# Performance work log

Measured on AMD Instinct MI355X. Metric: run time of the kernel, lower is better.

The kernel has to match this reference:

```python
import jax, jax.numpy as jnp
import numpy as np

N_NODES = 50000
N_EDGES = 800000
IN_F = 128
HID_F = 128
OUT_F = 128

def safediv(a, b):
    b = jnp.where(b == 0, jnp.ones_like(b), b)
    return a / b

def setup_inputs() -> dict:
    key = jax.random.key(0)
    ks = jax.random.split(key, 8)
    h = jax.random.normal(ks[0], (N_NODES, IN_F), dtype=jnp.float32)
    ppr_weight = jax.random.uniform(ks[1], (N_EDGES,), dtype=jnp.float32)
    Qw = jax.random.normal(ks[2], (HID_F, IN_F), dtype=jnp.float32) * (1.0 / np.sqrt(IN_F))
    Qb = jnp.zeros((HID_F,), dtype=jnp.float32)
    Ww = jax.random.normal(ks[3], (OUT_F, IN_F + HID_F), dtype=jnp.float32) * (1.0 / np.sqrt(IN_F + HID_F))
    Wb = jnp.zeros((OUT_F,), dtype=jnp.float32)
    src = jax.random.randint(ks[4], (N_EDGES,), 0, N_NODES, dtype=jnp.int64 if jax.config.jax_enable_x64 else jnp.int32)
    dst = jax.random.randint(ks[5], (N_EDGES,), 0, N_NODES, dtype=jnp.int64 if jax.config.jax_enable_x64 else jnp.int32)
    return {"h": h, "ppr_weight": ppr_weight, "Qw": Qw, "Qb": Qb, "Ww": Ww, "Wb": Wb, "src": src, "dst": dst}

def reference(h, ppr_weight, Qw, Qb, Ww, Wb, src, dst):
    # neighbor transform: Q(h) -> [N, HID_F]
    hq = h @ Qw.T + Qb
    # message: h_w = hq[src] * ppr_weight  (edge-weighted gather) [E, HID_F]
    msg = hq[src] * ppr_weight[:, None]
    # reduce: scatter-sum messages and weights onto dst nodes
    h_agg = jax.ops.segment_sum(msg, dst, num_segments=N_NODES)
    w = jax.ops.segment_sum(ppr_weight, dst, num_segments=N_NODES)
    # apply: PPR-weighted mean, concat, linear, leaky_relu, L2 normalize
    h_agg = safediv(h_agg, w[:, None])
    h_concat = jnp.concatenate([h, h_agg], axis=1)
    h_new = jax.nn.leaky_relu(h_concat @ Ww.T + Wb, negative_slope=0.01)
    norm = jnp.linalg.norm(h_new, axis=1, keepdims=True)
    return safediv(h_new, norm)
```

## Files before the change

kernel.cpp:

```cpp
#include <hip/hip_runtime.h>
#include <stdint.h>

#define N_NODES 50000
#define N_EDGES 800000
#define IN_F 128
#define HID_F 128
#define OUT_F 128
#define CAT_F 256

#define NB 256
#define CHUNK 3136
#define NBUCK 3125
#define BCAP 384

typedef __bf16 bf16x8 __attribute__((ext_vector_type(8)));
typedef float f32x4 __attribute__((ext_vector_type(4)));

__device__ __forceinline__ uint32_t f2b(float f) {
  uint32_t u = __float_as_uint(f);
  return (u + 0x7fffu + ((u >> 16) & 1u)) >> 16;
}

__global__ void __launch_bounds__(256) prep_hist_kernel(
    const int* __restrict__ dst, int* __restrict__ G, const float* __restrict__ h,
    const float* __restrict__ Qw, const float* __restrict__ Ww, uint16_t* __restrict__ hB,
    uint16_t* __restrict__ QwB, uint16_t* __restrict__ WwB) {
  if (blockIdx.x < NB) {
    __shared__ int hist[NBUCK];
    for (int k = threadIdx.x; k < NBUCK; k += 256) hist[k] = 0;
    __syncthreads();
    int b = blockIdx.x;
    int base = b * CHUNK;
    int end = (base + CHUNK < N_EDGES) ? (base + CHUNK) : N_EDGES;
    for (int i4 = base / 4 + threadIdx.x; i4 * 4 < end; i4 += 256) {
      int4 d4 = ((const int4*)dst)[i4];
      atomicAdd(&hist[d4.x >> 4], 1);
      atomicAdd(&hist[d4.y >> 4], 1);
      atomicAdd(&hist[d4.z >> 4], 1);
      atomicAdd(&hist[d4.w >> 4], 1);
    }
    __syncthreads();
    for (int k = threadIdx.x; k < NBUCK; k += 256) G[(size_t)b * NBUCK + k] = hist[k];
  } else {
    const int TOT4 = (N_NODES * IN_F + HID_F * IN_F + OUT_F * CAT_F) / 4;
    int i4 = (blockIdx.x - NB) * 256 + threadIdx.x;
    if (i4 >= TOT4) return;
    int base = i4 * 4;
    const float* src;
    uint16_t* dstp;
    int off;
    if (base < N_NODES * IN_F) {
      src = h; dstp = hB; off = base;
    } else if (base < N_NODES * IN_F + HID_F * IN_F) {
      src = Qw; dstp = QwB; off = base - N_NODES * IN_F;
    } else {
      src = Ww; dstp = WwB; off = base - N_NODES * IN_F - HID_F * IN_F;
    }
    float4 v = *(const float4*)(src + off);
    ushort4 o;
    o.x = (uint16_t)f2b(v.x); o.y = (uint16_t)f2b(v.y);
    o.z = (uint16_t)f2b(v.z); o.w = (uint16_t)f2b(v.w);
    *(ushort4*)(dstp + off) = o;
  }
}

__global__ void __launch_bounds__(256) colscan_kernel(int* __restrict__ G,
                                                      int* __restrict__ Btot) {
  int w = (blockIdx.x * 256 + (int)threadIdx.x) >> 6;
  if (w >= NBUCK) return;
  int lane = threadIdx.x & 63;
  int v0 = G[(size_t)(4 * lane + 0) * NBUCK + w];
  int v1 = G[(size_t)(4 * lane + 1) * NBUCK + w];
  int v2 = G[(size_t)(4 * lane + 2) * NBUCK + w];
  int v3 = G[(size_t)(4 * lane + 3) * NBUCK + w];
  int s = v0 + v1 + v2 + v3;
  int inc = s;
#pragma unroll
  for (int d = 1; d < 64; d <<= 1) {
    int x = __shfl_up(inc, d, 64);
    if (lane >= d) inc += x;
  }
  int exc = inc - s;
  G[(size_t)(4 * lane + 0) * NBUCK + w] = exc;
  G[(size_t)(4 * lane + 1) * NBUCK + w] = exc + v0;
  G[(size_t)(4 * lane + 2) * NBUCK + w] = exc + v0 + v1;
  G[(size_t)(4 * lane + 3) * NBUCK + w] = exc + v0 + v1 + v2;
  if (lane == 63) Btot[w] = inc;
}

__global__ void base_scan_kernel(const int* __restrict__ Btot, int* __restrict__ Bbase) {
  int lane = threadIdx.x;
  int c[49], loc[49];
  int s = 0;
#pragma unroll
  for (int j = 0; j < 49; ++j) {
    int i = lane * 49 + j;
    c[j] = (i < NBUCK) ? Btot[i] : 0;
    loc[j] = s;
    s += c[j];
  }
  int inc = s;
#pragma unroll
  for (int d = 1; d < 64; d <<= 1) {
    int x = __shfl_up(inc, d, 64);
    if (lane >= d) inc += x;
  }
  int exc = inc - s;
#pragma unroll
  for (int j = 0; j < 49; ++j) {
    int i = lane * 49 + j;
    if (i <= NBUCK) Bbase[i] = exc + loc[j];
  }
}

__global__ void __launch_bounds__(256) scatter_kernel(
    const int* __restrict__ dst, const int* __restrict__ src, const float* __restrict__ ppr,
    const int* __restrict__ G, const int* __restrict__ Bbase, int2* __restrict__ rec) {
  __shared__ int cursor[NBUCK];
  int b = blockIdx.x;
  for (int k = threadIdx.x; k < NBUCK; k += 256)
    cursor[k] = Bbase[k] + G[(size_t)b * NBUCK + k];
  __syncthreads();
  int base = b * CHUNK;
  int end = (base + CHUNK < N_EDGES) ? (base + CHUNK) : N_EDGES;
  for (int i4 = base / 4 + threadIdx.x; i4 * 4 < end; i4 += 256) {
    int4 d4 = ((const int4*)dst)[i4];
    int4 s4 = ((const int4*)src)[i4];
    float4 w4 = ((const float4*)ppr)[i4];
    int p;
    p = atomicAdd(&cursor[d4.x >> 4], 1);
    rec[p] = make_int2(s4.x | ((d4.x & 15) << 20), __float_as_int(w4.x));
    p = atomicAdd(&cursor[d4.y >> 4], 1);
    rec[p] = make_int2(s4.y | ((d4.y & 15) << 20), __float_as_int(w4.y));
    p = atomicAdd(&cursor[d4.z >> 4], 1);
    rec[p] = make_int2(s4.z | ((d4.z & 15) << 20), __float_as_int(w4.z));
    p = atomicAdd(&cursor[d4.w >> 4], 1);
    rec[p] = make_int2(s4.w | ((d4.w & 15) << 20), __float_as_int(w4.w));
  }
}

__global__ void __launch_bounds__(256) agg_gemm2_kernel(
    const int2* __restrict__ rec, const int* __restrict__ Bbase,
    const uint16_t* __restrict__ hB, const uint16_t* __restrict__ QwB,
    const float* __restrict__ Qb, const uint16_t* __restrict__ WwB,
    const float* __restrict__ Wb, float* __restrict__ out) {
  __shared__ int2 srec[BCAP];
  __shared__ uint4 hagg[16][17];
  __shared__ uint4 hq2[16][17];
  __shared__ int hist[16];
  __shared__ int noff[17];
  __shared__ int cur[16];
  __shared__ float wsum[16];
  __shared__ float ssp[4][16];
  int g = blockIdx.x;
  int t = threadIdx.x;
  if (t < 16) hist[t] = 0;
  __syncthreads();

  int rbeg = Bbase[g];
  int len = Bbase[g + 1] - rbeg;
  len = (len < BCAP) ? len : BCAP;

  int2 rc[2];
#pragma unroll
  for (int k = 0; k < 2; ++k) {
    int i = t + k * 256;
    if (i < len) {
      rc[k] = rec[rbeg + i];
      atomicAdd(&hist[rc[k].x >> 20], 1);
    }
  }
  __syncthreads();

  if (t < 16) {
    int v = hist[t];
    int inc = v;
#pragma unroll
    for (int d = 1; d < 16; d <<= 1) {
      int x = __shfl_up(inc, d, 64);
      if (t >= d) inc += x;
    }
    noff[t] = inc - v;
    cur[t] = inc - v;
    if (t == 15) noff[16] = inc;
  }
  __syncthreads();

#pragma unroll
  for (int k = 0; k < 2; ++k) {
    int i = t + k * 256;
    if (i < len) {
      int p = atomicAdd(&cur[rc[k].x >> 20], 1);
      srec[p] = rc[k];
    }
  }
  __syncthreads();

  {
    int gs = t >> 4, c = t & 15;
    const uint4* hb4 = (const uint4*)hB;
    int nl = gs;
    int nbeg = noff[nl], nend = noff[nl + 1];
    int last = nend - 1;
    float a[8];
#pragma unroll
    for (int j = 0; j < 8; ++j) a[j] = 0.f;
    float ws = 0.f;

    int2 rrA[4], rrB[4];
    uint4 uA[4], uB[4];

#define LOADB(E0, RR, UU)                                         \
  {                                                               \
    _Pragma("unroll") for (int j = 0; j < 4; ++j) {               \
      int i = (E0) + j;                                           \
      RR[j] = srec[(i < last) ? i : last];                        \
    }                                                             \
    _Pragma("unroll") for (int j = 0; j < 4; ++j)                 \
        UU[j] = hb4[(size_t)(RR[j].x & 0xFFFFF) * 16 + c];        \
  }

#define CONSB(E0, RR, UU)                                           \
  {                                                                 \
    _Pragma("unroll") for (int j = 0; j < 4; ++j) {                 \
      float w = ((E0) + j < nend) ? __int_as_float(RR[j].y) : 0.f;  \
      ws += w;                                                      \
      uint32_t x;                                                   \
      x = UU[j].x;                                                  \
      a[0] += w * __uint_as_float(x << 16);                         \
      a[1] += w * __uint_as_float(x & 0xffff0000u);                 \
      x = UU[j].y;                                                  \
      a[2] += w * __uint_as_float(x << 16);                         \
      a[3] += w * __uint_as_float(x & 0xffff0000u);                 \
      x = UU[j].z;                                                  \
      a[4] += w * __uint_as_float(x << 16);                         \
      a[5] += w * __uint_as_float(x & 0xffff0000u);                 \
      x = UU[j].w;                                                  \
      a[6] += w * __uint_as_float(x << 16);                         \
      a[7] += w * __uint_as_float(x & 0xffff0000u);                 \
    }                                                               \
  }

    int e = nbeg;
    if (e < nend) {
      LOADB(e, rrA, uA);
      while (true) {
        int eB = e + 4;
        if (eB < nend) {
          LOADB(eB, rrB, uB);
          CONSB(e, rrA, uA);
          int eA = eB + 4;
          if (eA < nend) {
            LOADB(eA, rrA, uA);
            CONSB(eB, rrB, uB);
            e = eA;
          } else {
            CONSB(eB, rrB, uB);
            break;
          }
        } else {
          CONSB(e, rrA, uA);
          break;
        }
      }
    }
#undef LOADB
#undef CONSB

    float dnm = (ws == 0.f) ? 1.f : ws;
    float inv = 1.f / dnm;
    uint4 o;
    o.x = f2b(a[0] * inv) | (f2b(a[1] * inv) << 16);
    o.y = f2b(a[2] * inv) | (f2b(a[3] * inv) << 16);
    o.z = f2b(a[4] * inv) | (f2b(a[5] * inv) << 16);
    o.w = f2b(a[6] * inv) | (f2b(a[7] * inv) << 16);
    hagg[nl][c] = o;
    if (c == 0) wsum[nl] = ws;
  }
  __syncthreads();

  int lane = t & 63, wv = t >> 6;
  int r = lane & 15, qd = lane >> 4;

#pragma unroll
  for (int tq = 0; tq < 2; ++tq) {
    int tt = wv * 2 + tq;
    f32x4 acc = (f32x4){0.f, 0.f, 0.f, 0.f};
#pragma unroll
    for (int kt = 0; kt < 4; ++kt) {
      bf16x8 av = *(const bf16x8*)&hagg[r][kt * 4 + qd];
      bf16x8 b = *(const bf16x8*)(QwB + (tt * 16 + r) * IN_F + kt * 32 + qd * 8);
      acc = __builtin_amdgcn_mfma_f32_16x16x32_bf16(av, b, acc, 0, 0, 0);
    }
    float qb = Qb[tt * 16 + r];
#pragma unroll
    for (int rr2 = 0; rr2 < 4; ++rr2) {
      int row = qd * 4 + rr2;
      float flag = (wsum[row] != 0.f) ? 1.f : 0.f;
      ((uint16_t*)&hq2[row][0])[tt * 16 + r] = (uint16_t)f2b(acc[rr2] + qb * flag);
    }
  }
  __syncthreads();

  int row0 = g * 16;
  f32x4 acc2[2];
  acc2[0] = (f32x4){0.f, 0.f, 0.f, 0.f};
  acc2[1] = (f32x4){0.f, 0.f, 0.f, 0.f};
  const uint16_t* aRow = hB + (size_t)(row0 + r) * IN_F + qd * 8;
#pragma unroll
  for (int kt = 0; kt < 8; ++kt) {
    bf16x8 av;
    if (kt < 4) {
      av = *(const bf16x8*)(aRow + kt * 32);
    } else {
      av = *(const bf16x8*)&hq2[r][(kt - 4) * 4 + qd];
    }
#pragma unroll
    for (int tq = 0; tq < 2; ++tq) {
      int tt = wv * 2 + tq;
      bf16x8 b = *(const bf16x8*)(WwB + (tt * 16 + r) * CAT_F + kt * 32 + qd * 8);
      acc2[tq] = __builtin_amdgcn_mfma_f32_16x16x32_bf16(av, b, acc2[tq], 0, 0, 0);
    }
  }
  float lv[2][4];
  float ss[4] = {0.f, 0.f, 0.f, 0.f};
#pragma unroll
  for (int tq = 0; tq < 2; ++tq) {
    int tt = wv * 2 + tq;
    float wb = Wb[tt * 16 + r];
#pragma unroll
    for (int rr2 = 0; rr2 < 4; ++rr2) {
      float v = acc2[tq][rr2] + wb;
      v = (v >= 0.f) ? v : 0.01f * v;
      lv[tq][rr2] = v;
      ss[rr2] += v * v;
    }
  }
#pragma unroll
  for (int rr2 = 0; rr2 < 4; ++rr2) {
    float s = ss[rr2];
    s += __shfl_xor(s, 1);
    s += __shfl_xor(s, 2);
    s += __shfl_xor(s, 4);
    s += __shfl_xor(s, 8);
    ss[rr2] = s;
  }
  if (r == 0) {
#pragma unroll
    for (int rr2 = 0; rr2 < 4; ++rr2) ssp[wv][qd * 4 + rr2] = ss[rr2];
  }
  __syncthreads();
#pragma unroll
  for (int rr2 = 0; rr2 < 4; ++rr2) {
    int row = qd * 4 + rr2;
    float tot = ssp[0][row] + ssp[1][row] + ssp[2][row] + ssp[3][row];
    float nr = sqrtf(tot);
    float inv = (nr == 0.f) ? 1.f : (1.f / nr);
    float* orow = out + (size_t)(row0 + row) * OUT_F;
#pragma unroll
    for (int tq = 0; tq < 2; ++tq) {
      int tt = wv * 2 + tq;
      orow[tt * 16 + r] = lv[tq][rr2] * inv;
    }
  }
}

extern "C" void kernel_launch(void* const* d_in, const int* in_sizes, int n_in,
                              void* d_out, int out_size, void* d_ws, size_t ws_size,
                              hipStream_t stream) {
  const float* h = (const float*)d_in[0];
  const float* ppr = (const float*)d_in[1];
  const float* Qw = (const float*)d_in[2];
  const float* Qb = (const float*)d_in[3];
  const float* Ww = (const float*)d_in[4];
  const float* Wb = (const float*)d_in[5];
  const int* src = (const int*)d_in[6];
  const int* dst = (const int*)d_in[7];
  float* out = (float*)d_out;

  char* ws = (char*)d_ws;
  size_t o = 0;
  auto alloc = [&](size_t bytes) {
    void* p = ws + o;
    o = (o + bytes + 255) & ~(size_t)255;
    return p;
  };
  uint16_t* hB = (uint16_t*)alloc((size_t)N_NODES * IN_F * 2);
  uint16_t* QwB = (uint16_t*)alloc((size_t)HID_F * IN_F * 2);
  uint16_t* WwB = (uint16_t*)alloc((size_t)OUT_F * CAT_F * 2);
  int* G = (int*)alloc((size_t)NB * NBUCK * 4);
  int* Btot = (int*)alloc((size_t)NBUCK * 4);
  int* Bbase = (int*)alloc((size_t)(NBUCK + 1) * 4);
  int2* rec = (int2*)alloc((size_t)N_EDGES * 8);

  const int CONV_BLOCKS = ((N_NODES * IN_F + HID_F * IN_F + OUT_F * CAT_F) / 4 + 255) / 256;
  prep_hist_kernel<<<NB + CONV_BLOCKS, 256, 0, stream>>>(dst, G, h, Qw, Ww, hB, QwB, WwB);
  colscan_kernel<<<(NBUCK + 3) / 4, 256, 0, stream>>>(G, Btot);
  base_scan_kernel<<<1, 64, 0, stream>>>(Btot, Bbase);
  scatter_kernel<<<NB, 256, 0, stream>>>(dst, src, ppr, G, Bbase, rec);
  agg_gemm2_kernel<<<NBUCK, 256, 0, stream>>>(rec, Bbase, hB, QwB, Qb, WwB, Wb, out);
}
```

Baseline: 195.3 us.

## Replace global bucket prefix scan with fixed-capacity per-bucket slots

Removes the single-block base_scan kernel by giving each destination bucket a fixed BCAP-sized slot in the record buffer, so scatter cursors start at k*BCAP plus the per-block column offset. The aggregation kernel reads the bucket count directly and indexes its slot. Records past BCAP are dropped, as the aggregation kernel already clamped to BCAP. This saves one serial launch and its latency. The buffer grows and the launch bounds add an occupancy hint of 4.

After: 186.6 us. 4.4% less time.

```diff
diff --git a/kernel.cpp b/kernel.cpp
--- a/kernel.cpp
+++ b/kernel.cpp
@@ -46,17 +46,17 @@
     int i4 = (blockIdx.x - NB) * 256 + threadIdx.x;
     if (i4 >= TOT4) return;
     int base = i4 * 4;
-    const float* src;
+    const float* srcp;
     uint16_t* dstp;
     int off;
     if (base < N_NODES * IN_F) {
-      src = h; dstp = hB; off = base;
+      srcp = h; dstp = hB; off = base;
     } else if (base < N_NODES * IN_F + HID_F * IN_F) {
-      src = Qw; dstp = QwB; off = base - N_NODES * IN_F;
+      srcp = Qw; dstp = QwB; off = base - N_NODES * IN_F;
     } else {
-      src = Ww; dstp = WwB; off = base - N_NODES * IN_F - HID_F * IN_F;
-    }
-    float4 v = *(const float4*)(src + off);
+      srcp = Ww; dstp = WwB; off = base - N_NODES * IN_F - HID_F * IN_F;
+    }
+    float4 v = *(const float4*)(srcp + off);
     ushort4 o;
     o.x = (uint16_t)f2b(v.x); o.y = (uint16_t)f2b(v.y);
     o.z = (uint16_t)f2b(v.z); o.w = (uint16_t)f2b(v.w);
@@ -65,7 +65,7 @@
 }
 
 __global__ void __launch_bounds__(256) colscan_kernel(int* __restrict__ G,
-                                                      int* __restrict__ Btot) {
+                                                      int* __restrict__ cnt) {
   int w = (blockIdx.x * 256 + (int)threadIdx.x) >> 6;
   if (w >= NBUCK) return;
   int lane = threadIdx.x & 63;
@@ -85,41 +85,16 @@
   G[(size_t)(4 * lane + 1) * NBUCK + w] = exc + v0;
   G[(size_t)(4 * lane + 2) * NBUCK + w] = exc + v0 + v1;
   G[(size_t)(4 * lane + 3) * NBUCK + w] = exc + v0 + v1 + v2;
-  if (lane == 63) Btot[w] = inc;
-}
-
-__global__ void base_scan_kernel(const int* __restrict__ Btot, int* __restrict__ Bbase) {
-  int lane = threadIdx.x;
-  int c[49], loc[49];
-  int s = 0;
-#pragma unroll
-  for (int j = 0; j < 49; ++j) {
-    int i = lane * 49 + j;
-    c[j] = (i < NBUCK) ? Btot[i] : 0;
-    loc[j] = s;
-    s += c[j];
-  }
-  int inc = s;
-#pragma unroll
-  for (int d = 1; d < 64; d <<= 1) {
-    int x = __shfl_up(inc, d, 64);
-    if (lane >= d) inc += x;
-  }
-  int exc = inc - s;
-#pragma unroll
-  for (int j = 0; j < 49; ++j) {
-    int i = lane * 49 + j;
-    if (i <= NBUCK) Bbase[i] = exc + loc[j];
-  }
+  if (lane == 63) cnt[w] = inc;
 }
 
 __global__ void __launch_bounds__(256) scatter_kernel(
     const int* __restrict__ dst, const int* __restrict__ src, const float* __restrict__ ppr,
-    const int* __restrict__ G, const int* __restrict__ Bbase, int2* __restrict__ rec) {
+    const int* __restrict__ G, int2* __restrict__ rec) {
   __shared__ int cursor[NBUCK];
   int b = blockIdx.x;
   for (int k = threadIdx.x; k < NBUCK; k += 256)
-    cursor[k] = Bbase[k] + G[(size_t)b * NBUCK + k];
+    cursor[k] = k * BCAP + G[(size_t)b * NBUCK + k];
   __syncthreads();
   int base = b * CHUNK;
   int end = (base + CHUNK < N_EDGES) ? (base + CHUNK) : N_EDGES;
@@ -127,20 +102,20 @@
     int4 d4 = ((const int4*)dst)[i4];
     int4 s4 = ((const int4*)src)[i4];
     float4 w4 = ((const float4*)ppr)[i4];
-    int p;
-    p = atomicAdd(&cursor[d4.x >> 4], 1);
-    rec[p] = make_int2(s4.x | ((d4.x & 15) << 20), __float_as_int(w4.x));
-    p = atomicAdd(&cursor[d4.y >> 4], 1);
-    rec[p] = make_int2(s4.y | ((d4.y & 15) << 20), __float_as_int(w4.y));
-    p = atomicAdd(&cursor[d4.z >> 4], 1);
-    rec[p] = make_int2(s4.z | ((d4.z & 15) << 20), __float_as_int(w4.z));
-    p = atomicAdd(&cursor[d4.w >> 4], 1);
-    rec[p] = make_int2(s4.w | ((d4.w & 15) << 20), __float_as_int(w4.w));
-  }
-}
-
-__global__ void __launch_bounds__(256) agg_gemm2_kernel(
-    const int2* __restrict__ rec, const int* __restrict__ Bbase,
+    int k, p;
+    k = d4.x >> 4; p = atomicAdd(&cursor[k], 1);
+    if (p < (k + 1) * BCAP) rec[p] = make_int2(s4.x | ((d4.x & 15) << 20), __float_as_int(w4.x));
+    k = d4.y >> 4; p = atomicAdd(&cursor[k], 1);
+    if (p < (k + 1) * BCAP) rec[p] = make_int2(s4.y | ((d4.y & 15) << 20), __float_as_int(w4.y));
+    k = d4.z >> 4; p = atomicAdd(&cursor[k], 1);
+    if (p < (k + 1) * BCAP) rec[p] = make_int2(s4.z | ((d4.z & 15) << 20), __float_as_int(w4.z));
+    k = d4.w >> 4; p = atomicAdd(&cursor[k], 1);
+    if (p < (k + 1) * BCAP) rec[p] = make_int2(s4.w | ((d4.w & 15) << 20), __float_as_int(w4.w));
+  }
+}
+
+__global__ void __launch_bounds__(256, 4) agg_gemm2_kernel(
+    const int2* __restrict__ rec, const int* __restrict__ cnt,
     const uint16_t* __restrict__ hB, const uint16_t* __restrict__ QwB,
     const float* __restrict__ Qb, const uint16_t* __restrict__ WwB,
     const float* __restrict__ Wb, float* __restrict__ out) {
@@ -157,16 +132,16 @@
   if (t < 16) hist[t] = 0;
   __syncthreads();
 
-  int rbeg = Bbase[g];
-  int len = Bbase[g + 1] - rbeg;
+  int len = cnt[g];
   len = (len < BCAP) ? len : BCAP;
+  const int2* rbase = rec + (size_t)g * BCAP;
 
   int2 rc[2];
 #pragma unroll
   for (int k = 0; k < 2; ++k) {
     int i = t + k * 256;
     if (i < len) {
-      rc[k] = rec[rbeg + i];
+      rc[k] = rbase[i];
       atomicAdd(&hist[rc[k].x >> 20], 1);
     }
   }
@@ -389,14 +364,12 @@
   uint16_t* QwB = (uint16_t*)alloc((size_t)HID_F * IN_F * 2);
   uint16_t* WwB = (uint16_t*)alloc((size_t)OUT_F * CAT_F * 2);
   int* G = (int*)alloc((size_t)NB * NBUCK * 4);
-  int* Btot = (int*)alloc((size_t)NBUCK * 4);
-  int* Bbase = (int*)alloc((size_t)(NBUCK + 1) * 4);
-  int2* rec = (int2*)alloc((size_t)N_EDGES * 8);
+  int* cnt = (int*)alloc((size_t)NBUCK * 4);
+  int2* rec = (int2*)alloc((size_t)NBUCK * BCAP * 8);
 
   const int CONV_BLOCKS = ((N_NODES * IN_F + HID_F * IN_F + OUT_F * CAT_F) / 4 + 255) / 256;
   prep_hist_kernel<<<NB + CONV_BLOCKS, 256, 0, stream>>>(dst, G, h, Qw, Ww, hB, QwB, WwB);
-  colscan_kernel<<<(NBUCK + 3) / 4, 256, 0, stream>>>(G, Btot);
-  base_scan_kernel<<<1, 64, 0, stream>>>(Btot, Bbase);
-  scatter_kernel<<<NB, 256, 0, stream>>>(dst, src, ppr, G, Bbase, rec);
-  agg_gemm2_kernel<<<NBUCK, 256, 0, stream>>>(rec, Bbase, hB, QwB, Qb, WwB, Wb, out);
-}
+  colscan_kernel<<<(NBUCK + 3) / 4, 256, 0, stream>>>(G, cnt);
+  scatter_kernel<<<NB, 256, 0, stream>>>(dst, src, ppr, G, rec);
+  agg_gemm2_kernel<<<NBUCK, 256, 0, stream>>>(rec, cnt, hB, QwB, Qb, WwB, Wb, out);
+}
```
